# Optimization experiments

Measured on AMD Instinct MI355X. Metric: run time of the kernel, lower is better.

The kernel has to match this reference:

```python
import jax, jax.numpy as jnp
import numpy as np

B, N, E = 8, 20000, 320000
C, D, HOPS, HID, OUT = 128, 64, 4, 512, 256


def setup_inputs() -> dict:
    key = jax.random.key(0)
    ks = jax.random.split(key, 8)
    edge_index = jax.random.randint(ks[0], (B, 2, E), 0, N, dtype=jnp.int64 if jax.config.jax_enable_x64 else jnp.int32)
    perturb_one_hot = jax.random.uniform(ks[1], (C, N), dtype=jnp.float32)
    emb_table = jax.random.normal(ks[2], (C, D), dtype=jnp.float32) * 0.02
    W1 = jax.random.normal(ks[3], (HOPS * D, HID), dtype=jnp.float32) * 0.02
    b1 = jnp.zeros((HID,), jnp.float32)
    gamma = jnp.ones((HID,), jnp.float32)
    beta = jnp.zeros((HID,), jnp.float32)
    W2 = jax.random.normal(ks[4], (HID, OUT), dtype=jnp.float32) * 0.02
    b2 = jnp.zeros((OUT,), jnp.float32)
    return {"edge_index": edge_index, "num_nodes": N, "perturb_one_hot": perturb_one_hot,
            "emb_table": emb_table, "W1": W1, "b1": b1, "gamma": gamma, "beta": beta,
            "W2": W2, "b2": b2}


def reference(edge_index, num_nodes, perturb_one_hot, emb_table, W1, b1, gamma, beta, W2, b2):
    d = emb_table.shape[1]
    max_hop = W1.shape[0] // d
    # init_emb: one embedding row per gene (node), shared across all graphs
    idx = jnp.argmax(perturb_one_hot.T, axis=1)          # (N,) indices into cells
    init_emb = emb_table[idx]                             # (N, D)

    def spmm(ei, H):
        # A @ H with A[row, col] = 1 (binary COO adjacency)
        return jax.ops.segment_sum(H[ei[1]], ei[0], num_segments=num_nodes)

    spmm_b = jax.vmap(spmm, in_axes=(0, 0))               # over graphs
    Bn = edge_index.shape[0]
    H = jnp.broadcast_to(init_emb, (Bn,) + init_emb.shape)  # (B, N, D)
    hops = []
    for _ in range(max_hop):
        H = spmm_b(edge_index, H)
        hops.append(H)
    # stack hops on last axis then flatten -> matches torch.stack(dim=-1).reshape(N,-1)
    omega = jnp.stack(hops, axis=-1).reshape(Bn, num_nodes, max_hop * d)
    x = omega @ W1 + b1
    mu = jnp.mean(x, axis=-1, keepdims=True)
    var = jnp.var(x, axis=-1, keepdims=True)
    x = (x - mu) * jax.lax.rsqrt(var + 1e-5) * gamma + beta
    x = jax.nn.gelu(x, approximate=False)
    return x @ W2 + b2
```

## Files before the change

### kernel.cpp

```cpp
#include <hip/hip_runtime.h>
#include <math.h>

#define BG 8
#define NN 20000
#define EE 320000
#define CC 128
#define DD 64
#define NHOPS 4
#define HID 512
#define OUTD 256
#define MAXDEG 64

typedef __attribute__((ext_vector_type(8))) short short8;
typedef __attribute__((ext_vector_type(4))) short s16x4;
typedef __attribute__((ext_vector_type(4))) float f32x4;

__device__ __forceinline__ unsigned short f2bf(float f) {
    unsigned u = __float_as_uint(f);
    u += 0x7fffu + ((u >> 16) & 1u);
    return (unsigned short)(u >> 16);
}

__device__ __forceinline__ float bf2f(unsigned short u) {
    return __uint_as_float(((unsigned)u) << 16);
}

__device__ __forceinline__ int swz(int la) {
    return la ^ ((la >> 4) & 1) ^ (((la >> 3) & 1) << 1);
}


__global__ __launch_bounds__(256) void zero_kernel(int* __restrict__ p, int n) {
    int i = blockIdx.x * 256 + threadIdx.x;
    if (i < n) p[i] = 0;
}

__global__ __launch_bounds__(256) void argmax_kernel(const float* __restrict__ P, int* __restrict__ idx) {
    int n = blockIdx.x * 256 + threadIdx.x;
    if (n >= NN) return;
    float best = __builtin_nontemporal_load(&P[n]);
    int bi = 0;
    #pragma unroll 4
    for (int c = 1; c < CC; ++c) {
        float v = __builtin_nontemporal_load(&P[c * NN + n]);
        if (v > best) { best = v; bi = c; }
    }
    idx[n] = bi;
}

__global__ __launch_bounds__(256) void build_kernel(const int* __restrict__ ei, int* __restrict__ count,
                                                    int* __restrict__ colpad) {
    int i = blockIdx.x * 256 + threadIdx.x;
    int b = i / EE, e = i - b * EE;
    const int* eb = ei + (long)b * 2 * EE;
    int row = __builtin_nontemporal_load(&eb[e]);
    int col = __builtin_nontemporal_load(&eb[EE + e]);
    int pos = atomicAdd(&count[b * NN + row], 1);
    if (pos < MAXDEG) colpad[((long)b * NN + row) * MAXDEG + pos] = col;
}


__global__ __launch_bounds__(256) void spmm_first_kernel(const int* __restrict__ idx, const float* __restrict__ emb,
                                                         const int* __restrict__ count,
                                                         const int* __restrict__ colpad,
                                                         short* __restrict__ Hout) {
    int wave = threadIdx.x >> 6, lane = threadIdx.x & 63;
    int b = blockIdx.x & 7;
    int n = (blockIdx.x >> 3) * 4 + wave;
    int cnt = min(count[b * NN + n], MAXDEG);
    const int* cs = colpad + ((long)b * NN + n) * MAXDEG;
    int e4 = lane >> 4, d4 = lane & 15;
    f32x4 sum = (f32x4)(0.f);
    int j = e4;
    int col = (j < cnt) ? __builtin_nontemporal_load(&cs[j]) : 0;
    while (j < cnt) {
        int jn = j + 4;
        int coln = (jn < cnt) ? __builtin_nontemporal_load(&cs[jn]) : 0;
        int cell = idx[col];
        sum += *(const f32x4*)&emb[(size_t)cell * DD + d4 * 4];
        j = jn;
        col = coln;
    }
    #pragma unroll
    for (int i = 0; i < 4; ++i) {
        sum[i] += __shfl_xor(sum[i], 16, 64);
        sum[i] += __shfl_xor(sum[i], 32, 64);
    }
    if (lane < 16) {
        s16x4 o;
        #pragma unroll
        for (int i = 0; i < 4; ++i) o[i] = (short)f2bf(sum[i]);
        __builtin_nontemporal_store(o, (s16x4*)&Hout[((long)b * NN + n) * DD + d4 * 4]);
    }
}

__global__ __launch_bounds__(256) void spmm_kernel(const short* __restrict__ Hin,
                                                   const int* __restrict__ count,
                                                   const int* __restrict__ colpad, short* __restrict__ Hout) {
    int wave = threadIdx.x >> 6, lane = threadIdx.x & 63;
    int b = blockIdx.x & 7;
    int n = (blockIdx.x >> 3) * 4 + wave;
    int cnt = min(count[b * NN + n], MAXDEG);
    const short* hb = Hin + (long)b * (NN * DD);
    const int* cs = colpad + ((long)b * NN + n) * MAXDEG;
    int e8 = lane >> 3, d8 = lane & 7;
    float sum[8] = {0.f, 0.f, 0.f, 0.f, 0.f, 0.f, 0.f, 0.f};
    int j = e8;
    int col = (j < cnt) ? __builtin_nontemporal_load(&cs[j]) : 0;
    while (j < cnt) {
        int jn = j + 8;
        int coln = (jn < cnt) ? __builtin_nontemporal_load(&cs[jn]) : 0;
        short8 v = *(const short8*)&hb[(size_t)col * DD + d8 * 8];
        #pragma unroll
        for (int i = 0; i < 8; ++i) sum[i] += bf2f((unsigned short)v[i]);
        j = jn;
        col = coln;
    }
    #pragma unroll
    for (int i = 0; i < 8; ++i) {
        sum[i] += __shfl_xor(sum[i], 8, 64);
        sum[i] += __shfl_xor(sum[i], 16, 64);
        sum[i] += __shfl_xor(sum[i], 32, 64);
    }
    if (lane < 8) {
        short8 o;
        #pragma unroll
        for (int i = 0; i < 8; ++i) o[i] = (short)f2bf(sum[i]);
        __builtin_nontemporal_store(o, (short8*)&Hout[((long)b * NN + n) * DD + lane * 8]);
    }
}

__global__ __launch_bounds__(256) void pack_w1_kernel(const float* __restrict__ W1, short* __restrict__ w1p) {
    int i = blockIdx.x * 256 + threadIdx.x;
    int j = i & 7, la = (i >> 3) & 63, kb = (i >> 9) & 7, ct = i >> 12;
    int kp = kb * 32 + ((la >> 4) & 3) * 8 + j;
    int h = kp >> 6, d = kp & 63;
    int k = d * 4 + h;
    int col = ct * 16 + (la & 15);
    w1p[i] = (short)f2bf(W1[k * HID + col]);
}

__global__ __launch_bounds__(256) void pack_w2_kernel(const float* __restrict__ W2, short* __restrict__ w2p) {
    int i = blockIdx.x * 256 + threadIdx.x;
    int j = i & 7, la = (i >> 3) & 63, kb = (i >> 9) & 15, ct = i >> 13;
    int k = kb * 32 + ((la >> 4) & 3) * 8 + j;
    int col = ct * 16 + (la & 15);
    w2p[i] = (short)f2bf(W2[k * OUTD + col]);
}

__global__ __launch_bounds__(256, 4) void mlp_mfma_kernel(const short* __restrict__ H,
                                                          const short* __restrict__ w1p,
                                                          const float* __restrict__ b1,
                                                          const float* __restrict__ gamma,
                                                          const float* __restrict__ beta,
                                                          const short* __restrict__ w2p,
                                                          const float* __restrict__ b2, float* __restrict__ out) {
    __shared__ short buf[16384];
    __shared__ float s1a[32 * 4];
    __shared__ float s2a[32 * 4];
    const int t = threadIdx.x;
    const int w = t >> 6, l = t & 63;
    const int q = l >> 4, cl = l & 15;
    const int lF = swz(l);
    const long g0 = (long)blockIdx.x * 32;

    {
        const int rsub = l >> 3, oct = l & 7;
        #pragma unroll
        for (int i = 0; i < 4; ++i) {
            int task = i * 4 + w;
            int h = task >> 2, rg = task & 3;
            int r = rg * 8 + rsub;
            short8 frag = __builtin_nontemporal_load(
                (const short8*)&H[((long)h * (BG * NN) + g0 + r) * DD + oct * 8]);
            int kb = (h << 1) | (oct >> 2);
            int quad = oct & 3;
            int rt = r >> 4;
            int la = (r & 15) | (quad << 4);
            *(short8*)&buf[((rt * 8 + kb) * 64 + swz(la)) * 8] = frag;
        }
    }
    __syncthreads();

    f32x4 acc[2][8];
    #pragma unroll
    for (int rt = 0; rt < 2; ++rt)
        #pragma unroll
        for (int c = 0; c < 8; ++c) acc[rt][c] = (f32x4)(0.f);
    #pragma unroll 2
    for (int kb = 0; kb < 8; ++kb) {
        short8 a[2];
        #pragma unroll
        for (int rt = 0; rt < 2; ++rt) a[rt] = *(const short8*)&buf[((rt * 8 + kb) * 64 + lF) * 8];
        #pragma unroll
        for (int c = 0; c < 8; ++c) {
            const short8 bfr = *(const short8*)(w1p + (((size_t)(w * 8 + c) * 8 + kb) * 64 + l) * 8);
            #pragma unroll
            for (int rt = 0; rt < 2; ++rt)
                acc[rt][c] = __builtin_amdgcn_mfma_f32_16x16x32_bf16(a[rt], bfr, acc[rt][c], 0, 0, 0);
        }
    }

    {
        float b1v[8];
        #pragma unroll
        for (int c = 0; c < 8; ++c) b1v[c] = b1[(w * 8 + c) * 16 + cl];
        float s1[2][4], s2[2][4];
        #pragma unroll
        for (int rt = 0; rt < 2; ++rt)
            #pragma unroll
            for (int i = 0; i < 4; ++i) {
                float a = 0.f, bb = 0.f;
                #pragma unroll
                for (int c = 0; c < 8; ++c) {
                    float x = acc[rt][c][i] + b1v[c];
                    acc[rt][c][i] = x;
                    a += x;
                    bb += x * x;
                }
                s1[rt][i] = a;
                s2[rt][i] = bb;
            }
        #pragma unroll
        for (int m = 1; m < 16; m <<= 1)
            #pragma unroll
            for (int rt = 0; rt < 2; ++rt)
                #pragma unroll
                for (int i = 0; i < 4; ++i) {
                    s1[rt][i] += __shfl_xor(s1[rt][i], m, 64);
                    s2[rt][i] += __shfl_xor(s2[rt][i], m, 64);
                }
        if (cl == 0) {
            #pragma unroll
            for (int rt = 0; rt < 2; ++rt)
                #pragma unroll
                for (int i = 0; i < 4; ++i) {
                    int row = rt * 16 + q * 4 + i;
                    s1a[row * 4 + w] = s1[rt][i];
                    s2a[row * 4 + w] = s2[rt][i];
                }
        }
    }
    __syncthreads();

    {
        float gv[8], bv[8];
        #pragma unroll
        for (int c = 0; c < 8; ++c) {
            int col = (w * 8 + c) * 16 + cl;
            gv[c] = gamma[col];
            bv[c] = beta[col];
        }
        #pragma unroll
        for (int rt = 0; rt < 2; ++rt)
            #pragma unroll
            for (int i = 0; i < 4; ++i) {
                int row = rt * 16 + q * 4 + i;
                float a = s1a[row * 4] + s1a[row * 4 + 1] + s1a[row * 4 + 2] + s1a[row * 4 + 3];
                float bb = s2a[row * 4] + s2a[row * 4 + 1] + s2a[row * 4 + 2] + s2a[row * 4 + 3];
                float mu = a * (1.f / HID);
                float var = bb * (1.f / HID) - mu * mu;
                float rs = rsqrtf(var + 1e-5f);
                #pragma unroll
                for (int c = 0; c < 8; ++c) {
                    int col = (w * 8 + c) * 16 + cl;
                    int kb2 = col >> 5, quad2 = (col >> 3) & 3, j2 = col & 7;
                    float x = (acc[rt][c][i] - mu) * rs * gv[c] + bv[c];
                    float g = 0.5f * x * (1.f + erff(x * 0.70710678118654752f));
                    int la = swz((q * 4 + i) | (quad2 << 4));
                    buf[((rt * 16 + kb2) * 64 + la) * 8 + j2] = (short)f2bf(g);
                }
            }
    }
    __syncthreads();

    f32x4 acc2[2][4];
    #pragma unroll
    for (int rt = 0; rt < 2; ++rt)
        #pragma unroll
        for (int c = 0; c < 4; ++c) acc2[rt][c] = (f32x4)(0.f);
    #pragma unroll 2
    for (int kb = 0; kb < 16; ++kb) {
        short8 a[2];
        #pragma unroll
        for (int rt = 0; rt < 2; ++rt) a[rt] = *(const short8*)&buf[((rt * 16 + kb) * 64 + lF) * 8];
        #pragma unroll
        for (int c = 0; c < 4; ++c) {
            const short8 bfr = *(const short8*)(w2p + (((size_t)(w * 4 + c) * 16 + kb) * 64 + l) * 8);
            #pragma unroll
            for (int rt = 0; rt < 2; ++rt)
                acc2[rt][c] = __builtin_amdgcn_mfma_f32_16x16x32_bf16(a[rt], bfr, acc2[rt][c], 0, 0, 0);
        }
    }

    float b2v[4];
    #pragma unroll
    for (int c = 0; c < 4; ++c) b2v[c] = b2[(w * 4 + c) * 16 + cl];
    #pragma unroll
    for (int rt = 0; rt < 2; ++rt)
        #pragma unroll
        for (int c = 0; c < 4; ++c)
            #pragma unroll
            for (int i = 0; i < 4; ++i) {
                long g = g0 + rt * 16 + q * 4 + i;
                __builtin_nontemporal_store(acc2[rt][c][i] + b2v[c],
                                            &out[g * OUTD + (w * 4 + c) * 16 + cl]);
            }
}


extern "C" void kernel_launch(void* const* d_in, const int* in_sizes, int n_in, void* d_out, int out_size,
                              void* d_ws, size_t ws_size, hipStream_t stream) {
    const int* ei = (const int*)d_in[0];
    const float* P = (const float*)d_in[2];
    const float* emb = (const float*)d_in[3];
    const float* W1 = (const float*)d_in[4];
    const float* b1 = (const float*)d_in[5];
    const float* gamma = (const float*)d_in[6];
    const float* beta = (const float*)d_in[7];
    const float* W2 = (const float*)d_in[8];
    const float* b2 = (const float*)d_in[9];
    float* out = (float*)d_out;

    char* ws = (char*)d_ws;
    size_t off = 0;
    auto alloc = [&](size_t bytes) -> char* {
        char* p = ws + off;
        off += (bytes + 1023) & ~(size_t)1023;
        return p;
    };
    int* idx = (int*)alloc((size_t)NN * 4);
    int* count = (int*)alloc((size_t)BG * NN * 4);
    int* colpad = (int*)alloc((size_t)BG * NN * MAXDEG * 4);
    short* w1p = (short*)alloc((size_t)131072 * 2);
    short* w2p = (short*)alloc((size_t)131072 * 2);
    short* H = (short*)alloc((size_t)NHOPS * BG * NN * DD * 2);

    hipLaunchKernelGGL(zero_kernel, dim3((BG * NN + 255) / 256), dim3(256), 0, stream, count, BG * NN);
    hipLaunchKernelGGL(argmax_kernel, dim3((NN + 255) / 256), dim3(256), 0, stream, P, idx);
    hipLaunchKernelGGL(build_kernel, dim3(BG * EE / 256), dim3(256), 0, stream, ei, count, colpad);
    hipLaunchKernelGGL(pack_w1_kernel, dim3(512), dim3(256), 0, stream, W1, w1p);
    hipLaunchKernelGGL(pack_w2_kernel, dim3(512), dim3(256), 0, stream, W2, w2p);

    const long hs = (long)BG * NN * DD;
    hipLaunchKernelGGL(spmm_first_kernel, dim3(BG * NN / 4), dim3(256), 0, stream, idx, emb, count, colpad, H);
    for (int h = 1; h < NHOPS; ++h) {
        hipLaunchKernelGGL(spmm_kernel, dim3(BG * NN / 4), dim3(256), 0, stream, H + (long)(h - 1) * hs, count,
                           colpad, H + (long)h * hs);
    }
    hipLaunchKernelGGL(mlp_mfma_kernel, dim3(BG * NN / 32), dim3(256), 0, stream, H, w1p, b1, gamma, beta, w2p, b2,
                       out);
}
```

Baseline: 822.5 us.

## Split SpMM neighbor lists by source half into two cache-friendly passes

```diff
diff --git a/kernel.cpp b/kernel.cpp
--- a/kernel.cpp
+++ b/kernel.cpp
@@ -10,6 +10,7 @@
 #define HID 512
 #define OUTD 256
 #define MAXDEG 64
+#define HALFN 10000
 
 typedef __attribute__((ext_vector_type(8))) short short8;
 typedef __attribute__((ext_vector_type(4))) short s16x4;
@@ -57,6 +58,25 @@
     int col = __builtin_nontemporal_load(&eb[EE + e]);
     int pos = atomicAdd(&count[b * NN + row], 1);
     if (pos < MAXDEG) colpad[((long)b * NN + row) * MAXDEG + pos] = col;
+}
+
+__global__ __launch_bounds__(256) void part_kernel(const int* __restrict__ count, int* __restrict__ colpad,
+                                                   int* __restrict__ hoff) {
+    int wave = threadIdx.x >> 6, lane = threadIdx.x & 63;
+    int b = blockIdx.x & 7;
+    int n = (blockIdx.x >> 3) * 4 + wave;
+    int cnt = min(count[b * NN + n], MAXDEG);
+    int* cs = colpad + ((long)b * NN + n) * MAXDEG;
+    bool active = lane < cnt;
+    int col = active ? cs[lane] : 0;
+    bool lo = col < HALFN;
+    unsigned long long below = (1ull << lane) - 1ull;
+    unsigned long long m0 = __ballot(active && lo);
+    unsigned long long m1 = __ballot(active && !lo);
+    int c0 = __popcll(m0);
+    int pos = lo ? __popcll(m0 & below) : c0 + __popcll(m1 & below);
+    if (active) cs[pos] = col;
+    if (lane == 0) hoff[b * NN + n] = c0 | (cnt << 8);
 }
 
 
@@ -90,26 +110,31 @@
         s16x4 o;
         #pragma unroll
         for (int i = 0; i < 4; ++i) o[i] = (short)f2bf(sum[i]);
-        __builtin_nontemporal_store(o, (s16x4*)&Hout[((long)b * NN + n) * DD + d4 * 4]);
-    }
-}
-
-__global__ __launch_bounds__(256) void spmm_kernel(const short* __restrict__ Hin,
-                                                   const int* __restrict__ count,
-                                                   const int* __restrict__ colpad, short* __restrict__ Hout) {
+        *(s16x4*)&Hout[((long)b * NN + n) * DD + d4 * 4] = o;
+    }
+}
+
+template <int PASS>
+__global__ __launch_bounds__(256) void spmm_half_kernel(const short* __restrict__ Hin,
+                                                        const int* __restrict__ hoff,
+                                                        const int* __restrict__ colpad,
+                                                        short* __restrict__ Hout) {
     int wave = threadIdx.x >> 6, lane = threadIdx.x & 63;
     int b = blockIdx.x & 7;
     int n = (blockIdx.x >> 3) * 4 + wave;
-    int cnt = min(count[b * NN + n], MAXDEG);
+    int ho = hoff[b * NN + n];
+    int c0 = ho & 255, cnt = (ho >> 8) & 255;
+    int s = PASS ? c0 : 0;
+    int e = PASS ? cnt : c0;
     const short* hb = Hin + (long)b * (NN * DD);
     const int* cs = colpad + ((long)b * NN + n) * MAXDEG;
     int e8 = lane >> 3, d8 = lane & 7;
     float sum[8] = {0.f, 0.f, 0.f, 0.f, 0.f, 0.f, 0.f, 0.f};
-    int j = e8;
-    int col = (j < cnt) ? __builtin_nontemporal_load(&cs[j]) : 0;
-    while (j < cnt) {
+    int j = s + e8;
+    int col = (j < e) ? __builtin_nontemporal_load(&cs[j]) : 0;
+    while (j < e) {
         int jn = j + 8;
-        int coln = (jn < cnt) ? __builtin_nontemporal_load(&cs[jn]) : 0;
+        int coln = (jn < e) ? __builtin_nontemporal_load(&cs[jn]) : 0;
         short8 v = *(const short8*)&hb[(size_t)col * DD + d8 * 8];
         #pragma unroll
         for (int i = 0; i < 8; ++i) sum[i] += bf2f((unsigned short)v[i]);
@@ -124,9 +149,16 @@
     }
     if (lane < 8) {
         short8 o;
-        #pragma unroll
-        for (int i = 0; i < 8; ++i) o[i] = (short)f2bf(sum[i]);
-        __builtin_nontemporal_store(o, (short8*)&Hout[((long)b * NN + n) * DD + lane * 8]);
+        short* dst = (short*)&Hout[((long)b * NN + n) * DD + lane * 8];
+        if (PASS) {
+            short8 prev = *(const short8*)dst;
+            #pragma unroll
+            for (int i = 0; i < 8; ++i) o[i] = (short)f2bf(sum[i] + bf2f((unsigned short)prev[i]));
+        } else {
+            #pragma unroll
+            for (int i = 0; i < 8; ++i) o[i] = (short)f2bf(sum[i]);
+        }
+        *(short8*)dst = o;
     }
 }
 
@@ -331,6 +363,7 @@
     };
     int* idx = (int*)alloc((size_t)NN * 4);
     int* count = (int*)alloc((size_t)BG * NN * 4);
+    int* hoff = (int*)alloc((size_t)BG * NN * 4);
     int* colpad = (int*)alloc((size_t)BG * NN * MAXDEG * 4);
     short* w1p = (short*)alloc((size_t)131072 * 2);
     short* w2p = (short*)alloc((size_t)131072 * 2);
@@ -339,14 +372,17 @@
     hipLaunchKernelGGL(zero_kernel, dim3((BG * NN + 255) / 256), dim3(256), 0, stream, count, BG * NN);
     hipLaunchKernelGGL(argmax_kernel, dim3((NN + 255) / 256), dim3(256), 0, stream, P, idx);
     hipLaunchKernelGGL(build_kernel, dim3(BG * EE / 256), dim3(256), 0, stream, ei, count, colpad);
+    hipLaunchKernelGGL(part_kernel, dim3(BG * NN / 4), dim3(256), 0, stream, count, colpad, hoff);
     hipLaunchKernelGGL(pack_w1_kernel, dim3(512), dim3(256), 0, stream, W1, w1p);
     hipLaunchKernelGGL(pack_w2_kernel, dim3(512), dim3(256), 0, stream, W2, w2p);
 
     const long hs = (long)BG * NN * DD;
     hipLaunchKernelGGL(spmm_first_kernel, dim3(BG * NN / 4), dim3(256), 0, stream, idx, emb, count, colpad, H);
     for (int h = 1; h < NHOPS; ++h) {
-        hipLaunchKernelGGL(spmm_kernel, dim3(BG * NN / 4), dim3(256), 0, stream, H + (long)(h - 1) * hs, count,
-                           colpad, H + (long)h * hs);
+        hipLaunchKernelGGL(spmm_half_kernel<0>, dim3(BG * NN / 4), dim3(256), 0, stream, H + (long)(h - 1) * hs,
+                           hoff, colpad, H + (long)h * hs);
+        hipLaunchKernelGGL(spmm_half_kernel<1>, dim3(BG * NN / 4), dim3(256), 0, stream, H + (long)(h - 1) * hs,
+                           hoff, colpad, H + (long)h * hs);
     }
     hipLaunchKernelGGL(mlp_mfma_kernel, dim3(BG * NN / 32), dim3(256), 0, stream, H, w1p, b1, gamma, beta, w2p, b2,
                        out);
```

Result: slower. 945.6 us (+15.0%).
